# Optimization experiments

Hardware: AMD Instinct MI355X
Metric: run time of the kernel (lower is better)

The kernel has to match this reference:

```python
import jax, jax.numpy as jnp
import numpy as np

B, F, H, N, S = 1024, 256, 256, 128, 2
DEV_MIN, DEV_MAX = 0.001, 0.01
LOG2PI = float(np.log(2.0 * np.pi))  # k/2*log(2pi) with k=2


def setup_inputs() -> dict:
    key = jax.random.key(0)
    ks = jax.random.split(key, 16)
    d = {}
    d['latents'] = jax.random.normal(ks[0], (B, F), jnp.float32)
    d['realPoints'] = jax.random.uniform(ks[1], (B, 2), jnp.float32)
    d['predMu'] = jax.random.uniform(ks[2], (B, 2), jnp.float32)
    d['predScale'] = 0.01 + 0.05 * jax.random.uniform(ks[3], (B, 2), jnp.float32)
    d['eps'] = jax.random.normal(ks[4], (S, B * N, 2), jnp.float32)
    dims = [F] + [H] * 5
    for i in range(5):
        d[f'W{i}'] = jax.random.normal(ks[5 + i], (dims[i], dims[i + 1]), jnp.float32) / np.sqrt(dims[i])
        d[f'b{i}'] = jnp.zeros((dims[i + 1],), jnp.float32)
    d['Wp'] = jax.random.normal(ks[10], (N, H, 2), jnp.float32) / np.sqrt(H)
    d['bp'] = jnp.zeros((N, 2), jnp.float32)
    return d


def _mvn_logprob(x, mu, s):
    # diagonal 2D Gaussian log_prob; broadcasts over leading dims
    z = (x - mu) / s
    return -0.5 * jnp.sum(z * z, axis=-1) - jnp.sum(jnp.log(s), axis=-1) - LOG2PI


def reference(latents, realPoints, predMu, predScale, eps,
              W0, b0, W1, b1, W2, b2, W3, b3, W4, b4, Wp, bp):
    h = latents
    for W, b in ((W0, b0), (W1, b1), (W2, b2), (W3, b3), (W4, b4)):
        h = jax.nn.relu(h @ W + b)
    mu = 0.5 + jnp.einsum('bh,nhk->bnk', h, Wp) + bp          # (B, N, 2)
    Bn, Nn = mu.shape[0], mu.shape[1]
    dev = jnp.linspace(DEV_MIN, DEV_MAX, Nn)[:, None]          # (N, 1)
    scale = jnp.tile(dev, (Bn, 2))                             # (B*N, 2)
    muF = mu.reshape(Bn * Nn, 2)

    # real-points loss: log_prob of each real point under all N gaussians, sigmoid
    pts_real = jnp.repeat(realPoints, Nn, axis=0)              # (B*N, 2)
    realLoss = jax.nn.sigmoid(_mvn_logprob(pts_real, muF, scale).reshape(Bn, Nn))

    # reparameterized samples: (S, B*N, 2) -> (S*N, B, 2)
    sampled = muF + scale * eps
    sampled = sampled.reshape(S, Bn, Nn, 2).transpose(0, 2, 1, 3).reshape(S * Nn, Bn, 2)

    # discriminator lossA: log_prob under detached predicted dist, sigmoid(-x), MSLE vs 0.5
    pmD = jax.lax.stop_gradient(predMu)
    psD = jax.lax.stop_gradient(predScale)
    la = _mvn_logprob(sampled, pmD, psD)                       # (S*N, B)
    la = la.reshape(S, Nn, Bn).transpose(2, 1, 0)              # (B, N, S)
    la = jax.nn.sigmoid(-la)
    lossA = jnp.mean(jnp.square(jnp.log1p(0.5) - jnp.log1p(la)), axis=-1)  # (B, N)

    # discriminator lossB: all-pairs log_prob of samples under own gaussians
    # equivalent to tf.repeat(sampled, N, axis=-2) then log_prob against (B*N,) batch
    z = (sampled[:, :, None, :] - mu[None, :, :, :]) / dev     # (S*N, B, N, 2)
    lb = -0.5 * jnp.sum(z * z, axis=-1) - 2.0 * jnp.log(dev[:, 0]) - LOG2PI  # (S*N, B, N)
    lb = lb.reshape(S, Nn, Bn, Nn).transpose(2, 1, 0, 3)       # (B, N, S, N)
    sm = jax.nn.softmax(lb, axis=-1)
    idx = jnp.arange(Nn)[None, :, None, None]
    diag = jnp.take_along_axis(sm, idx, axis=-1)[..., 0]       # (B, N, S)
    lossB = jnp.square(1.0 - diag)

    # generator loss: log_prob of detached samples under (non-detached) predicted dist
    gl = _mvn_logprob(jax.lax.stop_gradient(sampled), predMu, predScale)  # (S*N, B)
    gl = jax.nn.sigmoid(gl).reshape(S, Nn, Bn).transpose(2, 1, 0)
    gl = jnp.mean(gl, axis=-1)                                 # (B, N)
    genLoss = gl * jax.lax.stop_gradient(1.0 - realLoss)

    return (sampled, genLoss, realLoss, lossA, lossB)
```

## Files before the change

### kernel.cpp

```cpp
#include <hip/hip_runtime.h>
#include <math.h>

#define BB   1024
#define HH   256
#define NN   128
#define SS   2
#define RR   4
#define LOG2PI_F 1.8378770664093453f
#define DEV_MIN_F 0.001f
#define DEV_STEP_F 7.08661417322835e-05f
#define LOG1P_HALF 0.40546510810816438f
#define SHIFT_F 12.0f

#define OFF_GEN  524288
#define OFF_REAL 655360
#define OFF_A    786432
#define OFF_B    917504

__global__ __launch_bounds__(256) void transpose_wp_kernel(
    const float* __restrict__ Wp, float* __restrict__ Wt) {
    const int k = blockIdx.x;
    const int j = threadIdx.x;
    Wt[k * 256 + j] = Wp[(j >> 1) * 512 + k * 2 + (j & 1)];
}

__device__ __forceinline__ void step8(float h0k, float h1k, float h2k, float h3k,
                                      float2 wv, float2& a0, float2& a1,
                                      float2& a2, float2& a3) {
    a0.x = fmaf(h0k, wv.x, a0.x); a0.y = fmaf(h0k, wv.y, a0.y);
    a1.x = fmaf(h1k, wv.x, a1.x); a1.y = fmaf(h1k, wv.y, a1.y);
    a2.x = fmaf(h2k, wv.x, a2.x); a2.y = fmaf(h2k, wv.y, a2.y);
    a3.x = fmaf(h3k, wv.x, a3.x); a3.y = fmaf(h3k, wv.y, a3.y);
}

#define CONSUME(BANK, HOFF)                                                    \
    {                                                                          \
        _Pragma("unroll")                                                      \
        for (int k4 = 0; k4 < 16; k4 += 4) {                                   \
            float4 h0 = *(const float4*)&h0p[(HOFF) + k4];                     \
            float4 h1 = *(const float4*)&h1p[(HOFF) + k4];                     \
            float4 h2 = *(const float4*)&h2p[(HOFF) + k4];                     \
            float4 h3 = *(const float4*)&h3p[(HOFF) + k4];                     \
            step8(h0.x, h1.x, h2.x, h3.x, BANK[k4 + 0], acc0, acc1, acc2, acc3); \
            step8(h0.y, h1.y, h2.y, h3.y, BANK[k4 + 1], acc0, acc1, acc2, acc3); \
            step8(h0.z, h1.z, h2.z, h3.z, BANK[k4 + 2], acc0, acc1, acc2, acc3); \
            step8(h0.w, h1.w, h2.w, h3.w, BANK[k4 + 3], acc0, acc1, acc2, acc3); \
        }                                                                      \
    }

__global__ __launch_bounds__(1024, 4) void mlp_loss_kernel(
    const float* __restrict__ latents,
    const float* __restrict__ eps,
    const float* __restrict__ realPts,
    const float* __restrict__ predMu,
    const float* __restrict__ predScale,
    const float* __restrict__ W0, const float* __restrict__ b0,
    const float* __restrict__ W1, const float* __restrict__ b1,
    const float* __restrict__ W2, const float* __restrict__ b2,
    const float* __restrict__ W3, const float* __restrict__ b3,
    const float* __restrict__ W4, const float* __restrict__ b4,
    const float* __restrict__ Wt,
    const float* __restrict__ bp,
    float* __restrict__ out) {
    __shared__ float  hbuf[2][RR][256];
    __shared__ float  part[8][RR][256];
    __shared__ float2 sprm[NN];

    const int t  = threadIdx.x;
    const int q  = t >> 7;
    const int c  = t & 127;
    const int rL = t >> 8;
    const int j  = t & 255;
    const int brow = blockIdx.x * RR;

    if (t < NN) {
        float dv = DEV_MIN_F + (float)t * DEV_STEP_F;
        sprm[t] = make_float2(-0.5f / (dv * dv), -2.f * __logf(dv) - LOG2PI_F);
    }
    hbuf[0][rL][j] = latents[(brow + rL) * 256 + j];

    const int nL = j >> 1;
    const int sL = j & 1;
    const float2 epv = ((const float2*)eps)[sL * (BB * NN) + (brow + rL) * NN + nL];

    const float* Ws[6] = {W0, W1, W2, W3, W4, Wt};
    const float* bs_[6] = {b0, b1, b2, b3, b4, bp};

    float2 wA[16], wB[16];
    {
        const float2* p = (const float2*)W0 + q * 32 * 128 + c;
        #pragma unroll
        for (int i = 0; i < 16; ++i) wA[i] = p[i * 128];
    }
    __syncthreads();

    int cur = 0;
    #pragma unroll
    for (int layer = 0; layer < 6; ++layer) {
        {
            const float2* p = (const float2*)Ws[layer] + (q * 32 + 16) * 128 + c;
            #pragma unroll
            for (int i = 0; i < 16; ++i) wB[i] = p[i * 128];
        }
        const float* __restrict__ h0p = &hbuf[cur][0][q * 32];
        const float* __restrict__ h1p = &hbuf[cur][1][q * 32];
        const float* __restrict__ h2p = &hbuf[cur][2][q * 32];
        const float* __restrict__ h3p = &hbuf[cur][3][q * 32];
        float2 acc0 = {0.f, 0.f}, acc1 = {0.f, 0.f};
        float2 acc2 = {0.f, 0.f}, acc3 = {0.f, 0.f};

        CONSUME(wA, 0)
        if (layer < 5) {
            const float2* pn = (const float2*)Ws[layer + 1] + q * 32 * 128 + c;
            #pragma unroll
            for (int i = 0; i < 16; ++i) wA[i] = pn[i * 128];
        }
        CONSUME(wB, 16)

        ((float2*)&part[q][0][0])[c] = acc0;
        ((float2*)&part[q][1][0])[c] = acc1;
        ((float2*)&part[q][2][0])[c] = acc2;
        ((float2*)&part[q][3][0])[c] = acc3;
        __syncthreads();

        float val = 0.f;
        #pragma unroll
        for (int p = 0; p < 8; ++p) val += part[p][rL][j];
        val += bs_[layer][j];
        if (layer == 5) val += 0.5f;
        else            val = fmaxf(val, 0.f);
        hbuf[cur ^ 1][rL][j] = val;
        __syncthreads();
        cur ^= 1;
    }

    const float* __restrict__ muL = &hbuf[cur][rL][0];
    const int b = brow + rL;
    const int n = nL, s = sL;
    const float devn = DEV_MIN_F + (float)n * DEV_STEP_F;
    const float2 prn = sprm[n];

    const float mux = muL[2 * n], muy = muL[2 * n + 1];
    const float px = fmaf(devn, epv.x, mux);
    const float py = fmaf(devn, epv.y, muy);

    ((float2*)out)[(size_t)(s * NN + n) * BB + b] = make_float2(px, py);

    const float pmx = predMu[b * 2],    pmy = predMu[b * 2 + 1];
    const float psx = predScale[b * 2], psy = predScale[b * 2 + 1];
    const float rx  = realPts[b * 2],   ry  = realPts[b * 2 + 1];

    float sum0 = 0.f, sum1 = 0.f;
    #pragma unroll 4
    for (int m = 0; m < NN; m += 2) {
        float4 mm = *(const float4*)&muL[2 * m];
        float4 pr = *(const float4*)&sprm[m];
        float dx0 = px - mm.x, dy0 = py - mm.y;
        float lb0 = fmaf(fmaf(dx0, dx0, dy0 * dy0), pr.x, pr.y);
        sum0 += __expf(lb0 - SHIFT_F);
        float dx1 = px - mm.z, dy1 = py - mm.w;
        float lb1 = fmaf(fmaf(dx1, dx1, dy1 * dy1), pr.z, pr.w);
        sum1 += __expf(lb1 - SHIFT_F);
    }
    float dxd = devn * epv.x, dyd = devn * epv.y;
    float lbd = fmaf(fmaf(dxd, dxd, dyd * dyd), prn.x, prn.y);
    float ed  = __expf(lbd - SHIFT_F);
    float diag = ed / (sum0 + sum1);
    float lbv = (1.f - diag) * (1.f - diag);
    out[OFF_B + (size_t)b * (NN * SS) + j] = lbv;

    float zx = (px - pmx) / psx, zy = (py - pmy) / psy;
    float la = -0.5f * (zx * zx + zy * zy) - __logf(psx) - __logf(psy) - LOG2PI_F;
    float aa = 1.f / (1.f + __expf(la));
    float termA = LOG1P_HALF - log1pf(aa);
    termA = termA * termA;
    float gg = 1.f / (1.f + __expf(-la));

    float drx = rx - mux, dry = ry - muy;
    float lr = fmaf(fmaf(drx, drx, dry * dry), prn.x, prn.y);
    float rl = 1.f / (1.f + __expf(-lr));

    float termA_sum = termA + __shfl_xor(termA, 1);
    float gg_sum    = gg + __shfl_xor(gg, 1);
    if (s == 0) {
        out[OFF_GEN  + (size_t)b * NN + n] = 0.5f * gg_sum * (1.f - rl);
        out[OFF_REAL + (size_t)b * NN + n] = rl;
        out[OFF_A    + (size_t)b * NN + n] = 0.5f * termA_sum;
    }
}

extern "C" void kernel_launch(void* const* d_in, const int* in_sizes, int n_in,
                              void* d_out, int out_size, void* d_ws, size_t ws_size,
                              hipStream_t stream) {
    const float* latents   = (const float*)d_in[0];
    const float* realPts   = (const float*)d_in[1];
    const float* predMu    = (const float*)d_in[2];
    const float* predScale = (const float*)d_in[3];
    const float* eps       = (const float*)d_in[4];
    const float* W0 = (const float*)d_in[5];
    const float* b0 = (const float*)d_in[6];
    const float* W1 = (const float*)d_in[7];
    const float* b1 = (const float*)d_in[8];
    const float* W2 = (const float*)d_in[9];
    const float* b2 = (const float*)d_in[10];
    const float* W3 = (const float*)d_in[11];
    const float* b3 = (const float*)d_in[12];
    const float* W4 = (const float*)d_in[13];
    const float* b4 = (const float*)d_in[14];
    const float* Wp = (const float*)d_in[15];
    const float* bp = (const float*)d_in[16];

    float* Wtp = (float*)d_ws;

    transpose_wp_kernel<<<dim3(256), dim3(256), 0, stream>>>(Wp, Wtp);
    mlp_loss_kernel<<<dim3(BB / RR), dim3(1024), 0, stream>>>(
        latents, eps, realPts, predMu, predScale,
        W0, b0, W1, b1, W2, b2, W3, b3, W4, b4, Wtp, bp, (float*)d_out);
}
```

Baseline: 125.9 us.

## Software-pipeline weight loads with inline asm and triple-buffered register banks

Replaces the two-bank weight prefetch with a triple-buffered stream of 8-row register banks. Loads are issued through inline global_load_dwordx2 asm, and explicit s_waitcnt vmcnt gates keep two banks in flight across layer boundaries. Biases and per-row scalars are preloaded into LDS and registers at the start, and barriers wait only on lgkmcnt rather than full __syncthreads. This aims to hide global memory latency in the MLP loop. It risks breaking if the compiler's own vmcnt accounting conflicts with the asm loads.

Measured after the change: 125.5 us. Within noise of the previous version (-0.3%).

```diff
diff --git a/kernel.cpp b/kernel.cpp
--- a/kernel.cpp
+++ b/kernel.cpp
@@ -17,6 +17,31 @@
 #define OFF_A    786432
 #define OFF_B    917504
 
+#define GLD2(dst, ptr, OFS) \
+    asm volatile("global_load_dwordx2 %0, %1, off offset:" OFS \
+                 : "=v"(dst) : "v"(ptr))
+
+#define LOADBANK(S, P)                                            \
+    {                                                             \
+        const float* _pp = (P);                                   \
+        GLD2(S[0], _pp, "-4096"); GLD2(S[1], _pp, "-3072");       \
+        GLD2(S[2], _pp, "-2048"); GLD2(S[3], _pp, "-1024");       \
+        GLD2(S[4], _pp, "0");     GLD2(S[5], _pp, "1024");        \
+        GLD2(S[6], _pp, "2048");  GLD2(S[7], _pp, "3072");        \
+    }
+
+#define GATEN(S, CNT)                                                      \
+    asm volatile("s_waitcnt vmcnt(" CNT ")"                                \
+                 : "+v"(S[0]), "+v"(S[1]), "+v"(S[2]), "+v"(S[3]),         \
+                   "+v"(S[4]), "+v"(S[5]), "+v"(S[6]), "+v"(S[7]))
+
+#define BAR_LDS()                                                 \
+    {                                                             \
+        asm volatile("s_waitcnt lgkmcnt(0)" ::: "memory");        \
+        __builtin_amdgcn_s_barrier();                             \
+        asm volatile("" ::: "memory");                            \
+    }
+
 __global__ __launch_bounds__(256) void transpose_wp_kernel(
     const float* __restrict__ Wp, float* __restrict__ Wt) {
     const int k = blockIdx.x;
@@ -24,46 +49,20 @@
     Wt[k * 256 + j] = Wp[(j >> 1) * 512 + k * 2 + (j & 1)];
 }
 
-__device__ __forceinline__ void step8(float h0k, float h1k, float h2k, float h3k,
-                                      float2 wv, float2& a0, float2& a1,
-                                      float2& a2, float2& a3) {
-    a0.x = fmaf(h0k, wv.x, a0.x); a0.y = fmaf(h0k, wv.y, a0.y);
-    a1.x = fmaf(h1k, wv.x, a1.x); a1.y = fmaf(h1k, wv.y, a1.y);
-    a2.x = fmaf(h2k, wv.x, a2.x); a2.y = fmaf(h2k, wv.y, a2.y);
-    a3.x = fmaf(h3k, wv.x, a3.x); a3.y = fmaf(h3k, wv.y, a3.y);
-}
-
-#define CONSUME(BANK, HOFF)                                                    \
-    {                                                                          \
-        _Pragma("unroll")                                                      \
-        for (int k4 = 0; k4 < 16; k4 += 4) {                                   \
-            float4 h0 = *(const float4*)&h0p[(HOFF) + k4];                     \
-            float4 h1 = *(const float4*)&h1p[(HOFF) + k4];                     \
-            float4 h2 = *(const float4*)&h2p[(HOFF) + k4];                     \
-            float4 h3 = *(const float4*)&h3p[(HOFF) + k4];                     \
-            step8(h0.x, h1.x, h2.x, h3.x, BANK[k4 + 0], acc0, acc1, acc2, acc3); \
-            step8(h0.y, h1.y, h2.y, h3.y, BANK[k4 + 1], acc0, acc1, acc2, acc3); \
-            step8(h0.z, h1.z, h2.z, h3.z, BANK[k4 + 2], acc0, acc1, acc2, acc3); \
-            step8(h0.w, h1.w, h2.w, h3.w, BANK[k4 + 3], acc0, acc1, acc2, acc3); \
-        }                                                                      \
-    }
-
 __global__ __launch_bounds__(1024, 4) void mlp_loss_kernel(
-    const float* __restrict__ latents,
-    const float* __restrict__ eps,
-    const float* __restrict__ realPts,
-    const float* __restrict__ predMu,
+    const float* __restrict__ latents, const float* __restrict__ eps,
+    const float* __restrict__ realPts, const float* __restrict__ predMu,
     const float* __restrict__ predScale,
     const float* __restrict__ W0, const float* __restrict__ b0,
     const float* __restrict__ W1, const float* __restrict__ b1,
     const float* __restrict__ W2, const float* __restrict__ b2,
     const float* __restrict__ W3, const float* __restrict__ b3,
     const float* __restrict__ W4, const float* __restrict__ b4,
-    const float* __restrict__ Wt,
-    const float* __restrict__ bp,
+    const float* __restrict__ Wt, const float* __restrict__ bp,
     float* __restrict__ out) {
     __shared__ float  hbuf[2][RR][256];
     __shared__ float  part[8][RR][256];
+    __shared__ float  sbias[6][256];
     __shared__ float2 sprm[NN];
 
     const int t  = threadIdx.x;
@@ -78,64 +77,87 @@
         sprm[t] = make_float2(-0.5f / (dv * dv), -2.f * __logf(dv) - LOG2PI_F);
     }
     hbuf[0][rL][j] = latents[(brow + rL) * 256 + j];
-
-    const int nL = j >> 1;
-    const int sL = j & 1;
-    const float2 epv = ((const float2*)eps)[sL * (BB * NN) + (brow + rL) * NN + nL];
-
-    const float* Ws[6] = {W0, W1, W2, W3, W4, Wt};
-    const float* bs_[6] = {b0, b1, b2, b3, b4, bp};
-
-    float2 wA[16], wB[16];
-    {
-        const float2* p = (const float2*)W0 + q * 32 * 128 + c;
-        #pragma unroll
-        for (int i = 0; i < 16; ++i) wA[i] = p[i * 128];
-    }
-    __syncthreads();
-
-    int cur = 0;
     #pragma unroll
-    for (int layer = 0; layer < 6; ++layer) {
-        {
-            const float2* p = (const float2*)Ws[layer] + (q * 32 + 16) * 128 + c;
-            #pragma unroll
-            for (int i = 0; i < 16; ++i) wB[i] = p[i * 128];
+    for (int ii = 0; ii < 2; ++ii) {
+        int idx = t + ii * 1024;
+        if (idx < 1536) {
+            int Lb = idx >> 8, jj = idx & 255;
+            const float* bsrc = (Lb == 0) ? b0 : (Lb == 1) ? b1 : (Lb == 2) ? b2
+                              : (Lb == 3) ? b3 : (Lb == 4) ? b4 : bp;
+            sbias[Lb][jj] = bsrc[jj];
         }
-        const float* __restrict__ h0p = &hbuf[cur][0][q * 32];
-        const float* __restrict__ h1p = &hbuf[cur][1][q * 32];
-        const float* __restrict__ h2p = &hbuf[cur][2][q * 32];
-        const float* __restrict__ h3p = &hbuf[cur][3][q * 32];
+    }
+    const int nL = j >> 1, sL = j & 1;
+    const int b = brow + rL;
+    const float2 epv = ((const float2*)eps)[sL * (BB * NN) + b * NN + nL];
+    const float2 pm  = ((const float2*)predMu)[b];
+    const float2 ps  = ((const float2*)predScale)[b];
+    const float2 rp  = ((const float2*)realPts)[b];
+
+    BAR_LDS();
+
+    const float* Wsrc[6] = {W0, W1, W2, W3, W4, Wt};
+    const int coff = 2 * c + 1024;
+
+    float2 bk[3][8];
+    LOADBANK(bk[0], W0 + (q * 32 + 0) * 256 + coff);
+    LOADBANK(bk[1], W0 + (q * 32 + 8) * 256 + coff);
+
+    #pragma unroll
+    for (int L = 0; L < 6; ++L) {
+        const int cur = L & 1;
         float2 acc0 = {0.f, 0.f}, acc1 = {0.f, 0.f};
         float2 acc2 = {0.f, 0.f}, acc3 = {0.f, 0.f};
-
-        CONSUME(wA, 0)
-        if (layer < 5) {
-            const float2* pn = (const float2*)Ws[layer + 1] + q * 32 * 128 + c;
+        #pragma unroll
+        for (int i = 0; i < 4; ++i) {
+            const int gb = L * 4 + i;
+            const int nb = gb + 2;
+            if (nb < 24) {
+                LOADBANK(bk[nb % 3],
+                         Wsrc[nb >> 2] + (q * 32 + (nb & 3) * 8) * 256 + coff);
+            }
+            if (gb <= 21)      { GATEN(bk[gb % 3], "16"); }
+            else if (gb == 22) { GATEN(bk[gb % 3], "8");  }
+            else               { GATEN(bk[gb % 3], "0");  }
+            const int kb = q * 32 + i * 8;
+            float4 hA0 = *(const float4*)&hbuf[cur][0][kb];
+            float4 hB0 = *(const float4*)&hbuf[cur][0][kb + 4];
+            float4 hA1 = *(const float4*)&hbuf[cur][1][kb];
+            float4 hB1 = *(const float4*)&hbuf[cur][1][kb + 4];
+            float4 hA2 = *(const float4*)&hbuf[cur][2][kb];
+            float4 hB2 = *(const float4*)&hbuf[cur][2][kb + 4];
+            float4 hA3 = *(const float4*)&hbuf[cur][3][kb];
+            float4 hB3 = *(const float4*)&hbuf[cur][3][kb + 4];
+            const float2* S = bk[gb % 3];
             #pragma unroll
-            for (int i = 0; i < 16; ++i) wA[i] = pn[i * 128];
+            for (int kk = 0; kk < 8; ++kk) {
+                float2 wv = S[kk];
+                float h0 = (kk < 4) ? (&hA0.x)[kk] : (&hB0.x)[kk - 4];
+                float h1 = (kk < 4) ? (&hA1.x)[kk] : (&hB1.x)[kk - 4];
+                float h2 = (kk < 4) ? (&hA2.x)[kk] : (&hB2.x)[kk - 4];
+                float h3 = (kk < 4) ? (&hA3.x)[kk] : (&hB3.x)[kk - 4];
+                acc0.x = fmaf(h0, wv.x, acc0.x); acc0.y = fmaf(h0, wv.y, acc0.y);
+                acc1.x = fmaf(h1, wv.x, acc1.x); acc1.y = fmaf(h1, wv.y, acc1.y);
+                acc2.x = fmaf(h2, wv.x, acc2.x); acc2.y = fmaf(h2, wv.y, acc2.y);
+                acc3.x = fmaf(h3, wv.x, acc3.x); acc3.y = fmaf(h3, wv.y, acc3.y);
+            }
         }
-        CONSUME(wB, 16)
-
         ((float2*)&part[q][0][0])[c] = acc0;
         ((float2*)&part[q][1][0])[c] = acc1;
         ((float2*)&part[q][2][0])[c] = acc2;
         ((float2*)&part[q][3][0])[c] = acc3;
-        __syncthreads();
-
+        BAR_LDS();
         float val = 0.f;
         #pragma unroll
         for (int p = 0; p < 8; ++p) val += part[p][rL][j];
-        val += bs_[layer][j];
-        if (layer == 5) val += 0.5f;
-        else            val = fmaxf(val, 0.f);
+        val += sbias[L][j];
+        if (L == 5) val += 0.5f;
+        else        val = fmaxf(val, 0.f);
         hbuf[cur ^ 1][rL][j] = val;
-        __syncthreads();
-        cur ^= 1;
-    }
-
-    const float* __restrict__ muL = &hbuf[cur][rL][0];
-    const int b = brow + rL;
+        BAR_LDS();
+    }
+
+    const float* __restrict__ muL = &hbuf[0][rL][0];
     const int n = nL, s = sL;
     const float devn = DEV_MIN_F + (float)n * DEV_STEP_F;
     const float2 prn = sprm[n];
@@ -145,10 +167,6 @@
     const float py = fmaf(devn, epv.y, muy);
 
     ((float2*)out)[(size_t)(s * NN + n) * BB + b] = make_float2(px, py);
-
-    const float pmx = predMu[b * 2],    pmy = predMu[b * 2 + 1];
-    const float psx = predScale[b * 2], psy = predScale[b * 2 + 1];
-    const float rx  = realPts[b * 2],   ry  = realPts[b * 2 + 1];
 
     float sum0 = 0.f, sum1 = 0.f;
     #pragma unroll 4
@@ -169,14 +187,14 @@
     float lbv = (1.f - diag) * (1.f - diag);
     out[OFF_B + (size_t)b * (NN * SS) + j] = lbv;
 
-    float zx = (px - pmx) / psx, zy = (py - pmy) / psy;
-    float la = -0.5f * (zx * zx + zy * zy) - __logf(psx) - __logf(psy) - LOG2PI_F;
+    float zx = (px - pm.x) / ps.x, zy = (py - pm.y) / ps.y;
+    float la = -0.5f * (zx * zx + zy * zy) - __logf(ps.x) - __logf(ps.y) - LOG2PI_F;
     float aa = 1.f / (1.f + __expf(la));
     float termA = LOG1P_HALF - log1pf(aa);
     termA = termA * termA;
     float gg = 1.f / (1.f + __expf(-la));
 
-    float drx = rx - mux, dry = ry - muy;
+    float drx = rp.x - mux, dry = rp.y - muy;
     float lr = fmaf(fmaf(drx, drx, dry * dry), prn.x, prn.y);
     float rl = 1.f / (1.f + __expf(-lr));
 
```
